# Performance work log

Hardware: AMD Instinct MI355X
Metric: run time of the kernel (lower is better)

The kernel has to match this reference:

```python
import jax, jax.numpy as jnp
import numpy as np

D_MODEL = 1024
N_HEADS = 16
D_K = D_MODEL // N_HEADS


def setup_inputs() -> dict:
    key = jax.random.key(0)
    kx, kq, kk, kv, ko = jax.random.split(key, 5)
    scale = 1.0 / np.sqrt(D_MODEL)
    return {
        "x": jax.random.normal(kx, (2, 2048, D_MODEL), dtype=jnp.float32),
        "W_Q": jax.random.normal(kq, (D_MODEL, D_MODEL), dtype=jnp.float32) * scale,
        "W_K": jax.random.normal(kk, (D_MODEL, D_MODEL), dtype=jnp.float32) * scale,
        "W_V": jax.random.normal(kv, (D_MODEL, D_MODEL), dtype=jnp.float32) * scale,
        "W_O": jax.random.normal(ko, (D_MODEL, D_MODEL), dtype=jnp.float32) * scale,
    }


def reference(x, W_Q, W_K, W_V, W_O) -> jnp.ndarray:
    B, S, _ = x.shape
    # Projections; weights stored as (d_model, d_model), applied as x @ W (Linear weight transposed convention folded into init)
    def heads(w):
        return jnp.einsum('bsd,de->bse', x, w).reshape(B, S, N_HEADS, D_K).transpose(0, 2, 1, 3)
    Q, K, V = heads(W_Q), heads(W_K), heads(W_V)  # (B,H,S,d_k)
    scores = jnp.einsum('bhqd,bhkd->bhqk', Q, K) / jnp.sqrt(jnp.asarray(D_K, x.dtype))
    causal_mask = jnp.triu(jnp.ones((S, S), dtype=bool), k=1)  # True above diagonal
    scores = jnp.where(causal_mask[None, None], jnp.asarray(-jnp.inf, x.dtype), scores)
    attn = jax.nn.softmax(scores, axis=-1)
    out = jnp.einsum('bhqk,bhkd->bhqd', attn, V)  # (B,H,S,d_k)
    out = out.transpose(0, 2, 1, 3).reshape(B, S, N_HEADS * D_K)
    return jnp.einsum('bsd,de->bse', out, W_O)
```

## Files before the change

### kernel.cpp

```cpp
#include <hip/hip_runtime.h>

typedef unsigned short u16;
typedef unsigned int u32;
typedef __attribute__((ext_vector_type(8))) __bf16 bf16x8;
typedef __attribute__((ext_vector_type(2))) __bf16 bf16x2;
typedef __attribute__((ext_vector_type(4))) float f32x4;
typedef __attribute__((ext_vector_type(16))) float f32x16;
typedef __attribute__((ext_vector_type(4))) u32 u32x4;

__device__ inline u16 f2bf(float f) {
  unsigned u = __builtin_bit_cast(unsigned, f);
  u += 0x7FFFu + ((u >> 16) & 1u);
  return (u16)(u >> 16);
}

__device__ inline u32 packbf(float a, float b) {
  bf16x2 t;
  t[0] = (__bf16)a;
  t[1] = (__bf16)b;
  return __builtin_bit_cast(u32, t);
}

__device__ inline void async16(const void* g, void* l) {
  __builtin_amdgcn_global_load_lds((const __attribute__((address_space(1))) void*)g,
                                   (__attribute__((address_space(3))) void*)l, 16, 0, 0);
}

__global__ __launch_bounds__(256) void xconv(const float* __restrict__ x, u16* __restrict__ xb) {
  int i = blockIdx.x * 256 + threadIdx.x;
  float4 v = ((const float4*)x)[i];
  ushort4 r;
  r.x = f2bf(v.x); r.y = f2bf(v.y); r.z = f2bf(v.z); r.w = f2bf(v.w);
  ((ushort4*)xb)[i] = r;
}

__global__ __launch_bounds__(256) void wtrans4(const float* __restrict__ W0,
                                               const float* __restrict__ W1,
                                               const float* __restrict__ W2,
                                               const float* __restrict__ W3,
                                               u16* __restrict__ WtQKV,
                                               u16* __restrict__ WtO) {
  __shared__ u16 tile[32][33];
  const int z = blockIdx.z;
  const float* W = (z == 0) ? W0 : (z == 1) ? W1 : (z == 2) ? W2 : W3;
  u16* Wt = (z < 3) ? (WtQKV + (size_t)z * 1024 * 1024) : WtO;
  const float s = (z == 0) ? 0.18033688011112042f : 1.0f;
  const int e0 = blockIdx.x * 32;
  const int d0 = blockIdx.y * 32;
  const int tx = threadIdx.x & 31;
  const int ty = threadIdx.x >> 5;
#pragma unroll
  for (int i = ty; i < 32; i += 8)
    tile[i][tx] = f2bf(W[(size_t)(d0 + i) * 1024 + e0 + tx] * s);
  __syncthreads();
#pragma unroll
  for (int i = ty; i < 32; i += 8)
    Wt[(size_t)(e0 + i) * 1024 + d0 + tx] = tile[tx][i];
}

__global__ __launch_bounds__(256) void vtrans(const u16* __restrict__ QKV, u16* __restrict__ Vtg) {
  __shared__ u16 t[32][66];
  const int tid = threadIdx.x;
  const int s0 = blockIdx.x * 32, dg0 = blockIdx.y * 64, b = blockIdx.z;
  {
    const int i = tid >> 3, c = (tid & 7) * 8;
    uint4 v = *(const uint4*)(QKV + (size_t)(b * 2048 + s0 + i) * 3072 + 2048 + dg0 + c);
    u16 tmp[8];
    *(uint4*)tmp = v;
#pragma unroll
    for (int e = 0; e < 8; ++e) t[i][c + e] = tmp[e];
  }
  __syncthreads();
  {
    const int r = tid >> 2, cg = (tid & 3) * 8;
    u16 tmp[8];
#pragma unroll
    for (int e = 0; e < 8; ++e) tmp[e] = t[cg + e][r];
    *(uint4*)(Vtg + (size_t)(b * 1024 + dg0 + r) * 2048 + s0 + cg) = *(uint4*)tmp;
  }
}

template <int OUT_BF16>
__global__ __launch_bounds__(256) void gemm_bt(const u16* __restrict__ A,
                                               const u16* __restrict__ Bt,
                                               void* __restrict__ Cp,
                                               int M, int N, int K) {
  __shared__ __align__(16) u16 As[128 * 32];
  __shared__ __align__(16) u16 Bs[128 * 32];
  const int tid = threadIdx.x;
  const int lane = tid & 63;
  const int wave = tid >> 6;
  const int lr = lane & 15;
  const int lk = (lane >> 4) * 8;
  const int wm = (wave >> 1) * 64;
  const int wn = (wave & 1) * 64;
  const int bm = blockIdx.x * 128;
  const int bn = blockIdx.y * 128;
  const int srow = lane >> 2;
  const int scol = (lane & 3) * 8;

  f32x4 acc[4][4] = {};

  for (int k0 = 0; k0 < K; k0 += 32) {
#pragma unroll
    for (int r = 0; r < 2; ++r) {
      const int chunk = r * 4 + wave;
      const int row = chunk * 16 + srow;
      async16(A + (size_t)(bm + row) * K + k0 + scol, &As[chunk * 512 + lane * 8]);
      async16(Bt + (size_t)(bn + row) * K + k0 + scol, &Bs[chunk * 512 + lane * 8]);
    }
    __syncthreads();
    bf16x8 a[4], b[4];
#pragma unroll
    for (int i = 0; i < 4; ++i) {
      a[i] = *(const bf16x8*)&As[(wm + i * 16 + lr) * 32 + lk];
      b[i] = *(const bf16x8*)&Bs[(wn + i * 16 + lr) * 32 + lk];
    }
#pragma unroll
    for (int mi = 0; mi < 4; ++mi)
#pragma unroll
      for (int ni = 0; ni < 4; ++ni)
        acc[mi][ni] = __builtin_amdgcn_mfma_f32_16x16x32_bf16(a[mi], b[ni], acc[mi][ni], 0, 0, 0);
    __syncthreads();
  }

#pragma unroll
  for (int mi = 0; mi < 4; ++mi) {
#pragma unroll
    for (int ni = 0; ni < 4; ++ni) {
      const int col = bn + wn + ni * 16 + lr;
#pragma unroll
      for (int j = 0; j < 4; ++j) {
        const int row = bm + wm + mi * 16 + (lane >> 4) * 4 + j;
        if (OUT_BF16)
          ((u16*)Cp)[(size_t)row * N + col] = f2bf(acc[mi][ni][j]);
        else
          ((float*)Cp)[(size_t)row * N + col] = acc[mi][ni][j];
      }
    }
  }
}

__global__ __launch_bounds__(256) void attn_kernel(const u16* __restrict__ QKV,
                                                   const u16* __restrict__ Vtg,
                                                   u16* __restrict__ Obuf) {
  constexpr int S = 2048, LD = 3072;
  __shared__ __align__(16) u16 Ks[2][64 * 64];
  __shared__ __align__(16) u16 Vs[64 * 64];

  const int qt = 15 - blockIdx.x;
  const int bh = blockIdx.y;
  const int b = bh >> 4, h = bh & 15;
  const int tid = threadIdx.x, lane = tid & 63, wave = tid >> 6;
  const int l31 = lane & 31, lh = lane >> 5;

  const int qbase = qt * 128 + wave * 32;

  const u16* qrow = QKV + (size_t)(b * S + qbase + l31) * LD + h * 64;
  bf16x8 qf[4];
#pragma unroll
  for (int c = 0; c < 4; ++c) qf[c] = *(const bf16x8*)(qrow + c * 16 + lh * 8);

  const int c0 = tid, c1 = tid + 256;
  const int r0 = c0 >> 3, x0 = ((c0 & 7) ^ (r0 & 7)) << 3;
  const int r1 = c1 >> 3, x1 = ((c1 & 7) ^ (r1 & 7)) << 3;
  const u16* Kbase = QKV + (size_t)b * S * LD + 1024 + h * 64;
  const u16* Vbase = Vtg + (size_t)bh * 64 * 2048;

  f32x16 o0 = {}, o1 = {};
  float m_run = -1e30f, l_run = 0.f;

  const int nkt = 2 * qt + 2;
  const int ktlast = qbase >> 6;

  async16(Kbase + (size_t)r0 * LD + x0, &Ks[0][c0 * 8]);
  async16(Kbase + (size_t)r1 * LD + x1, &Ks[0][c1 * 8]);
  __syncthreads();

  int cur = 0;
  for (int kt = 0; kt < nkt; ++kt) {
    const bool haveNext = (kt + 1 < nkt);
    async16(Vbase + (size_t)r0 * 2048 + kt * 64 + x0, &Vs[c0 * 8]);
    async16(Vbase + (size_t)r1 * 2048 + kt * 64 + x1, &Vs[c1 * 8]);
    if (haveNext) {
      async16(Kbase + (size_t)((kt + 1) * 64 + r0) * LD + x0, &Ks[cur ^ 1][c0 * 8]);
      async16(Kbase + (size_t)((kt + 1) * 64 + r1) * LD + x1, &Ks[cur ^ 1][c1 * 8]);
    }

    const bool active = (kt <= ktlast);
    const bool hiA = active && ((kt < ktlast) || (wave & 1));

    f32x16 t0 = {}, t1 = {};
    u32 pk0[8], pk1[8], sw0[8], sw1[8];

    if (active) {
      const u16* ks = Ks[cur];
      __builtin_amdgcn_s_setprio(1);
#pragma unroll
      for (int c = 0; c < 4; ++c) {
        const int cc = 2 * c + lh;
        const bf16x8 kf0 = *(const bf16x8*)&ks[l31 * 64 + ((cc ^ (l31 & 7)) << 3)];
        t0 = __builtin_amdgcn_mfma_f32_32x32x16_bf16(kf0, qf[c], t0, 0, 0, 0);
        if (hiA) {
          const bf16x8 kf1 = *(const bf16x8*)&ks[(32 + l31) * 64 + ((cc ^ (l31 & 7)) << 3)];
          t1 = __builtin_amdgcn_mfma_f32_32x32x16_bf16(kf1, qf[c], t1, 0, 0, 0);
        }
      }
      __builtin_amdgcn_s_setprio(0);

      if (kt == ktlast) {
        const int kb = kt * 64 + 4 * lh;
        const int qa = qbase + l31;
#pragma unroll
        for (int r = 0; r < 16; ++r) {
          const int ko = (r & 3) + 8 * (r >> 2);
          if (kb + ko > qa) t0[r] = -3e38f;
          if (hiA && (kb + 32 + ko > qa)) t1[r] = -3e38f;
        }
      }

      float u[16];
#pragma unroll
      for (int r = 0; r < 16; ++r) u[r] = hiA ? fmaxf(t0[r], t1[r]) : t0[r];
#pragma unroll
      for (int s = 8; s >= 1; s >>= 1)
#pragma unroll
        for (int r = 0; r < s; ++r) u[r] = fmaxf(u[r], u[r + s]);
      const float mx = fmaxf(u[0], __shfl_xor(u[0], 32));

      if (__any(mx > m_run + 8.0f)) {
        const float mnew = fmaxf(m_run, mx);
        const float scl = exp2f(m_run - mnew);
        m_run = mnew;
        l_run *= scl;
#pragma unroll
        for (int r = 0; r < 16; ++r) {
          const float sq = __shfl(scl, ((r & 3) + 8 * (r >> 2)) + 4 * lh);
          o0[r] *= sq;
          o1[r] *= sq;
        }
      }

#pragma unroll
      for (int r = 0; r < 16; ++r) t0[r] = exp2f(t0[r] - m_run);
      if (hiA) {
#pragma unroll
        for (int r = 0; r < 16; ++r) t1[r] = exp2f(t1[r] - m_run);
      }
      float v[16];
#pragma unroll
      for (int r = 0; r < 16; ++r) v[r] = hiA ? (t0[r] + t1[r]) : t0[r];
#pragma unroll
      for (int s = 8; s >= 1; s >>= 1)
#pragma unroll
        for (int r = 0; r < s; ++r) v[r] += v[r + s];
      l_run += v[0] + __shfl_xor(v[0], 32);

#pragma unroll
      for (int j = 0; j < 8; ++j) pk0[j] = packbf(t0[2 * j], t0[2 * j + 1]);
#pragma unroll
      for (int j = 0; j < 8; ++j) sw0[j] = __shfl_xor(pk0[j], 32);
      if (hiA) {
#pragma unroll
        for (int j = 0; j < 8; ++j) pk1[j] = packbf(t1[2 * j], t1[2 * j + 1]);
#pragma unroll
        for (int j = 0; j < 8; ++j) sw1[j] = __shfl_xor(pk1[j], 32);
      }
    }

    if (haveNext) asm volatile("s_waitcnt vmcnt(2)" ::: "memory");
    else          asm volatile("s_waitcnt vmcnt(0)" ::: "memory");
    __builtin_amdgcn_s_barrier();
    __builtin_amdgcn_sched_barrier(0);

    if (active) {
      __builtin_amdgcn_s_setprio(1);
#define PVSTEP(kc, pk, sw)                                                             \
      {                                                                                \
        const int q4 = ((kc) & 1) * 4;                                                 \
        u32x4 wv;                                                                      \
        wv[0] = lh ? sw[q4 + 2] : pk[q4 + 0];                                          \
        wv[1] = lh ? sw[q4 + 3] : pk[q4 + 1];                                          \
        wv[2] = lh ? pk[q4 + 2] : sw[q4 + 0];                                          \
        wv[3] = lh ? pk[q4 + 3] : sw[q4 + 1];                                          \
        const bf16x8 pa = __builtin_bit_cast(bf16x8, wv);                              \
        const int cc = 2 * (kc) + lh;                                                  \
        const bf16x8 vf0 = *(const bf16x8*)&Vs[l31 * 64 + ((cc ^ (l31 & 7)) << 3)];    \
        const bf16x8 vf1 = *(const bf16x8*)&Vs[(32 + l31) * 64 + ((cc ^ (l31 & 7)) << 3)]; \
        o0 = __builtin_amdgcn_mfma_f32_32x32x16_bf16(pa, vf0, o0, 0, 0, 0);            \
        o1 = __builtin_amdgcn_mfma_f32_32x32x16_bf16(pa, vf1, o1, 0, 0, 0);            \
      }
      PVSTEP(0, pk0, sw0)
      PVSTEP(1, pk0, sw0)
      if (hiA) {
        PVSTEP(2, pk1, sw1)
        PVSTEP(3, pk1, sw1)
      }
#undef PVSTEP
      __builtin_amdgcn_s_setprio(0);
    }

    __syncthreads();
    cur ^= 1;
  }

  const float linv = 1.0f / l_run;
#pragma unroll
  for (int r = 0; r < 16; ++r) {
    const int qo = (r & 3) + 8 * (r >> 2) + 4 * lh;
    const float lq = __shfl(linv, qo);
    u16* op = Obuf + (size_t)(b * S + qbase + qo) * 1024 + h * 64 + l31;
    op[0] = f2bf(o0[r] * lq);
    op[32] = f2bf(o1[r] * lq);
  }
}

extern "C" void kernel_launch(void* const* d_in, const int* in_sizes, int n_in,
                              void* d_out, int out_size, void* d_ws, size_t ws_size,
                              hipStream_t stream) {
  const float* x  = (const float*)d_in[0];
  const float* WQ = (const float*)d_in[1];
  const float* WK = (const float*)d_in[2];
  const float* WV = (const float*)d_in[3];
  const float* WO = (const float*)d_in[4];
  float* out = (float*)d_out;

  u16* xb    = (u16*)d_ws;
  u16* WtQKV = xb + (size_t)4096 * 1024;
  u16* WtO   = WtQKV + (size_t)3072 * 1024;
  u16* QKV   = WtO + (size_t)1024 * 1024;
  u16* Obuf  = QKV + (size_t)4096 * 3072;
  u16* Vtg   = Obuf + (size_t)4096 * 1024;

  xconv<<<4096, 256, 0, stream>>>(x, xb);
  wtrans4<<<dim3(32, 32, 4), 256, 0, stream>>>(WQ, WK, WV, WO, WtQKV, WtO);

  gemm_bt<1><<<dim3(32, 24), 256, 0, stream>>>(xb, WtQKV, QKV, 4096, 3072, 1024);
  vtrans<<<dim3(64, 16, 2), 256, 0, stream>>>(QKV, Vtg);
  attn_kernel<<<dim3(16, 32), 256, 0, stream>>>(QKV, Vtg, Obuf);
  gemm_bt<0><<<dim3(32, 8), 256, 0, stream>>>(Obuf, WtO, out, 4096, 1024, 1024);
}
```

Before: 170.6 us.

## Pair light and heavy causal query tiles per block and double-buffer V

Each block now handles two 64-row query tiles, a short one (pairIdx) and a long one (31-pairIdx), split between wave pairs. The goal is to even out causal-attention work across blocks instead of giving blocks widely different loads. V is now double-buffered alongside K, with both staged one tile ahead through a single macro. This removes the explicit vmcnt wait and mid-iteration barrier between the QK and PV phases. In exchange, the waves on the short tile sit idle through the rest of the block's longer loop, and LDS use grows with the second V buffer.

```diff
diff --git a/kernel.cpp b/kernel.cpp
--- a/kernel.cpp
+++ b/kernel.cpp
@@ -146,15 +146,19 @@
                                                    u16* __restrict__ Obuf) {
   constexpr int S = 2048, LD = 3072;
   __shared__ __align__(16) u16 Ks[2][64 * 64];
-  __shared__ __align__(16) u16 Vs[64 * 64];
-
-  const int qt = 15 - blockIdx.x;
+  __shared__ __align__(16) u16 Vs[2][64 * 64];
+
+  const int pairIdx = blockIdx.x;
   const int bh = blockIdx.y;
   const int b = bh >> 4, h = bh & 15;
   const int tid = threadIdx.x, lane = tid & 63, wave = tid >> 6;
   const int l31 = lane & 31, lh = lane >> 5;
 
-  const int qbase = qt * 128 + wave * 32;
+  const int tileA = pairIdx;
+  const int tileB = 31 - pairIdx;
+  const int myTile = (wave < 2) ? tileA : tileB;
+  const int qbase = myTile * 64 + (wave & 1) * 32;
+  const int ktlast = myTile;
 
   const u16* qrow = QKV + (size_t)(b * S + qbase + l31) * LD + h * 64;
   bf16x8 qf[4];
@@ -167,34 +171,34 @@
   const u16* Kbase = QKV + (size_t)b * S * LD + 1024 + h * 64;
   const u16* Vbase = Vtg + (size_t)bh * 64 * 2048;
 
+#define STAGE(buf, kt_)                                                          \
+  do {                                                                           \
+    async16(Kbase + (size_t)((kt_)*64 + r0) * LD + x0, &Ks[buf][c0 * 8]);        \
+    async16(Kbase + (size_t)((kt_)*64 + r1) * LD + x1, &Ks[buf][c1 * 8]);        \
+    async16(Vbase + (size_t)r0 * 2048 + (kt_)*64 + x0, &Vs[buf][c0 * 8]);        \
+    async16(Vbase + (size_t)r1 * 2048 + (kt_)*64 + x1, &Vs[buf][c1 * 8]);        \
+  } while (0)
+
   f32x16 o0 = {}, o1 = {};
   float m_run = -1e30f, l_run = 0.f;
 
-  const int nkt = 2 * qt + 2;
-  const int ktlast = qbase >> 6;
-
-  async16(Kbase + (size_t)r0 * LD + x0, &Ks[0][c0 * 8]);
-  async16(Kbase + (size_t)r1 * LD + x1, &Ks[0][c1 * 8]);
+  const int nkt = tileB + 1;
+
+  STAGE(0, 0);
   __syncthreads();
 
   int cur = 0;
   for (int kt = 0; kt < nkt; ++kt) {
-    const bool haveNext = (kt + 1 < nkt);
-    async16(Vbase + (size_t)r0 * 2048 + kt * 64 + x0, &Vs[c0 * 8]);
-    async16(Vbase + (size_t)r1 * 2048 + kt * 64 + x1, &Vs[c1 * 8]);
-    if (haveNext) {
-      async16(Kbase + (size_t)((kt + 1) * 64 + r0) * LD + x0, &Ks[cur ^ 1][c0 * 8]);
-      async16(Kbase + (size_t)((kt + 1) * 64 + r1) * LD + x1, &Ks[cur ^ 1][c1 * 8]);
-    }
+    if (kt + 1 < nkt) STAGE(cur ^ 1, kt + 1);
 
     const bool active = (kt <= ktlast);
     const bool hiA = active && ((kt < ktlast) || (wave & 1));
 
-    f32x16 t0 = {}, t1 = {};
-    u32 pk0[8], pk1[8], sw0[8], sw1[8];
-
     if (active) {
       const u16* ks = Ks[cur];
+      const u16* vs = Vs[cur];
+
+      f32x16 t0 = {}, t1 = {};
       __builtin_amdgcn_s_setprio(1);
 #pragma unroll
       for (int c = 0; c < 4; ++c) {
@@ -241,39 +245,34 @@
         }
       }
 
-#pragma unroll
-      for (int r = 0; r < 16; ++r) t0[r] = exp2f(t0[r] - m_run);
+      f32x16 p0 = t0, p1 = t1;
+#pragma unroll
+      for (int r = 0; r < 16; ++r) p0[r] = exp2f(t0[r] - m_run);
       if (hiA) {
 #pragma unroll
-        for (int r = 0; r < 16; ++r) t1[r] = exp2f(t1[r] - m_run);
+        for (int r = 0; r < 16; ++r) p1[r] = exp2f(t1[r] - m_run);
       }
       float v[16];
 #pragma unroll
-      for (int r = 0; r < 16; ++r) v[r] = hiA ? (t0[r] + t1[r]) : t0[r];
+      for (int r = 0; r < 16; ++r) v[r] = hiA ? (p0[r] + p1[r]) : p0[r];
 #pragma unroll
       for (int s = 8; s >= 1; s >>= 1)
 #pragma unroll
         for (int r = 0; r < s; ++r) v[r] += v[r + s];
       l_run += v[0] + __shfl_xor(v[0], 32);
 
-#pragma unroll
-      for (int j = 0; j < 8; ++j) pk0[j] = packbf(t0[2 * j], t0[2 * j + 1]);
+      u32 pk0[8], pk1[8], sw0[8], sw1[8];
+#pragma unroll
+      for (int j = 0; j < 8; ++j) pk0[j] = packbf(p0[2 * j], p0[2 * j + 1]);
 #pragma unroll
       for (int j = 0; j < 8; ++j) sw0[j] = __shfl_xor(pk0[j], 32);
       if (hiA) {
 #pragma unroll
-        for (int j = 0; j < 8; ++j) pk1[j] = packbf(t1[2 * j], t1[2 * j + 1]);
+        for (int j = 0; j < 8; ++j) pk1[j] = packbf(p1[2 * j], p1[2 * j + 1]);
 #pragma unroll
         for (int j = 0; j < 8; ++j) sw1[j] = __shfl_xor(pk1[j], 32);
       }
-    }
-
-    if (haveNext) asm volatile("s_waitcnt vmcnt(2)" ::: "memory");
-    else          asm volatile("s_waitcnt vmcnt(0)" ::: "memory");
-    __builtin_amdgcn_s_barrier();
-    __builtin_amdgcn_sched_barrier(0);
-
-    if (active) {
+
       __builtin_amdgcn_s_setprio(1);
 #define PVSTEP(kc, pk, sw)                                                             \
       {                                                                                \
@@ -285,8 +284,8 @@
         wv[3] = lh ? pk[q4 + 3] : sw[q4 + 1];                                          \
         const bf16x8 pa = __builtin_bit_cast(bf16x8, wv);                              \
         const int cc = 2 * (kc) + lh;                                                  \
-        const bf16x8 vf0 = *(const bf16x8*)&Vs[l31 * 64 + ((cc ^ (l31 & 7)) << 3)];    \
-        const bf16x8 vf1 = *(const bf16x8*)&Vs[(32 + l31) * 64 + ((cc ^ (l31 & 7)) << 3)]; \
+        const bf16x8 vf0 = *(const bf16x8*)&vs[l31 * 64 + ((cc ^ (l31 & 7)) << 3)];    \
+        const bf16x8 vf1 = *(const bf16x8*)&vs[(32 + l31) * 64 + ((cc ^ (l31 & 7)) << 3)]; \
         o0 = __builtin_amdgcn_mfma_f32_32x32x16_bf16(pa, vf0, o0, 0, 0, 0);            \
         o1 = __builtin_amdgcn_mfma_f32_32x32x16_bf16(pa, vf1, o1, 0, 0, 0);            \
       }
@@ -303,6 +302,7 @@
     __syncthreads();
     cur ^= 1;
   }
+#undef STAGE
 
   const float linv = 1.0f / l_run;
 #pragma unroll
```

Result: no change. 168.1 us (-1.5%).
